# Kernel tuning notes

Measured on AMD Instinct MI355X. Metric: run time of the kernel, lower is better.

The kernel has to match this reference:

```python
import jax, jax.numpy as jnp
import numpy as np

N_HEADS = 16
LN_EPS = 1e-5


def setup_inputs() -> dict:
    key = jax.random.key(0)
    k_z, k_qkv, k_proj = jax.random.split(key, 3)
    b, n, dm = 4, 2048, 1024
    z = jax.random.normal(k_z, (b, n, dm), dtype=jnp.float32)
    gamma = jnp.ones((dm,), dtype=jnp.float32)
    beta = jnp.zeros((dm,), dtype=jnp.float32)
    # parameterize Linear weights as (in, out) so y = x @ w (same math as torch x @ W.T)
    w_qkv = jax.random.normal(k_qkv, (dm, 3 * dm), dtype=jnp.float32) * (1.0 / np.sqrt(dm))
    w_proj = jax.random.normal(k_proj, (dm, dm), dtype=jnp.float32) * (1.0 / np.sqrt(dm))
    b_proj = jnp.zeros((dm,), dtype=jnp.float32)
    return {"z": z, "gamma": gamma, "beta": beta, "w_qkv": w_qkv,
            "w_proj": w_proj, "b_proj": b_proj}


def reference(z, gamma, beta, w_qkv, w_proj, b_proj):
    b, n, dm = z.shape
    h = N_HEADS
    d = dm // h
    scaling = jnp.asarray(np.sqrt(dm / h), dtype=z.dtype)

    # LayerNorm over last dim
    mu = jnp.mean(z, axis=-1, keepdims=True)
    var = jnp.mean(jnp.square(z - mu), axis=-1, keepdims=True)
    zn = (z - mu) * jax.lax.rsqrt(var + LN_EPS) * gamma + beta

    qkv = zn @ w_qkv  # [b, n, 3*dm]
    # einops 'b n (h d qkv_n) -> qkv_n b h n d': qkv index is INNERMOST of packed dim
    qkv = qkv.reshape(b, n, h, d, 3)
    q = qkv[..., 0]  # [b, n, h, d]
    k = qkv[..., 1]
    v = qkv[..., 2]

    scores = jnp.einsum('bqhd,bkhd->bhqk', q, k) / scaling  # [b, h, n, n]
    att = jax.nn.softmax(scores, axis=-1)
    out = jnp.einsum('bhqk,bkhd->bqhd', att, v).reshape(b, n, dm)
    out = out @ w_proj + b_proj  # projection (drop_hidden=False); dropout is identity in eval
    return z + out
```

## Files before the change

### kernel.cpp

```cpp
#include <hip/hip_runtime.h>

typedef unsigned short ushort;
typedef unsigned int uint;

typedef __bf16 bf16x8 __attribute__((ext_vector_type(8)));
typedef float floatx4 __attribute__((ext_vector_type(4)));

constexpr int BATCH = 4;
constexpr int SEQ = 2048;
constexpr int DM = 1024;
constexpr int NH = 16;
constexpr int HD = 64;
constexpr int M = BATCH * SEQ;
constexpr int NQKV = 3 * DM;
constexpr float QSCALE = 0.18033688011112042f;

__device__ __forceinline__ ushort f2b(float f) {
    uint x; __builtin_memcpy(&x, &f, 4);
    x += 0x7fffu + ((x >> 16) & 1u);
    return (ushort)(x >> 16);
}

__device__ __forceinline__ void gload16(const ushort* g, ushort* l) {
    __builtin_amdgcn_global_load_lds(
        (const __attribute__((address_space(1))) void*)g,
        (__attribute__((address_space(3))) void*)l, 16, 0, 0);
}

__global__ __launch_bounds__(256) void prep_kernel(
    const float* __restrict__ w_qkv, ushort* __restrict__ wqT,
    const float* __restrict__ w_proj, ushort* __restrict__ wpT,
    const float* __restrict__ z, const float* __restrict__ gamma,
    const float* __restrict__ beta, ushort* __restrict__ zn) {
    __shared__ ushort tile[64][65];
    int id = blockIdx.x;
    int t = threadIdx.x;
    if (id < 1024) {
        int tx = t & 63, ty = t >> 6;
        if (id < 768) {
            int bx = id % 48, by = id / 48;
            int c0 = bx * 64, r0 = by * 64;
#pragma unroll
            for (int i = 0; i < 64; i += 4)
                tile[i + ty][tx] = f2b(w_qkv[(size_t)(r0 + i + ty) * NQKV + c0 + tx]);
            __syncthreads();
#pragma unroll
            for (int i = 0; i < 64; i += 4) {
                int c = c0 + i + ty;
                int cp = (c % 3) * DM + c / 3;
                wqT[(size_t)cp * DM + r0 + tx] = tile[tx][i + ty];
            }
        } else {
            int q = id - 768;
            int c0 = (q % 16) * 64, r0 = (q / 16) * 64;
#pragma unroll
            for (int i = 0; i < 64; i += 4)
                tile[i + ty][tx] = f2b(w_proj[(size_t)(r0 + i + ty) * DM + c0 + tx]);
            __syncthreads();
#pragma unroll
            for (int i = 0; i < 64; i += 4)
                wpT[(size_t)(c0 + i + ty) * DM + r0 + tx] = tile[tx][i + ty];
        }
        return;
    }
    int row = id - 1024;
    float4 v = reinterpret_cast<const float4*>(z + (size_t)row * DM)[t];
    float s = v.x + v.y + v.z + v.w;
    float sq = v.x * v.x + v.y * v.y + v.z * v.z + v.w * v.w;
#pragma unroll
    for (int off = 32; off >= 1; off >>= 1) {
        s  += __shfl_xor(s, off);
        sq += __shfl_xor(sq, off);
    }
    __shared__ float red[8];
    int wave = t >> 6;
    if ((t & 63) == 0) { red[wave] = s; red[wave + 4] = sq; }
    __syncthreads();
    s  = red[0] + red[1] + red[2] + red[3];
    sq = red[4] + red[5] + red[6] + red[7];
    float mean = s * (1.f / DM);
    float var  = sq * (1.f / DM) - mean * mean;
    float rstd = rsqrtf(var + 1e-5f);
    float4 g = reinterpret_cast<const float4*>(gamma)[t];
    float4 bt = reinterpret_cast<const float4*>(beta)[t];
    ushort4 o;
    o.x = f2b((v.x - mean) * rstd * g.x + bt.x);
    o.y = f2b((v.y - mean) * rstd * g.y + bt.y);
    o.z = f2b((v.z - mean) * rstd * g.z + bt.z);
    o.w = f2b((v.w - mean) * rstd * g.w + bt.w);
    reinterpret_cast<ushort4*>(zn + (size_t)row * DM)[t] = o;
}

__device__ __forceinline__ void gemm128_core(
    const ushort* __restrict__ A, const ushort* __restrict__ BT,
    int m0, int n0, int t, floatx4 (&acc)[4][4],
    ushort (*As)[64], ushort (*Bs)[64]) {
    int lane = t & 63, w = t >> 6;
    int l16 = lane & 15, quad = lane >> 4;
    int wm = (w >> 1) * 64, wn = (w & 1) * 64;
#pragma unroll
    for (int i = 0; i < 4; i++)
#pragma unroll
        for (int j = 0; j < 4; j++) acc[i][j] = (floatx4){0.f, 0.f, 0.f, 0.f};

    int srow8 = lane >> 3;
    int lseg = (lane & 7) ^ srow8;
    const ushort* gA[4]; const ushort* gB[4];
    ushort* lA[4]; ushort* lB[4];
#pragma unroll
    for (int c = 0; c < 4; c++) {
        int r = 32 * c + 8 * w + srow8;
        gA[c] = &A [(size_t)(m0 + r) * DM + lseg * 8];
        gB[c] = &BT[(size_t)(n0 + r) * DM + lseg * 8];
        lA[c] = &As[32 * c + 8 * w][0];
        lB[c] = &Bs[32 * c + 8 * w][0];
    }
    int sw = l16 & 7;

    for (int k0 = 0; k0 < DM; k0 += 64) {
#pragma unroll
        for (int c = 0; c < 4; c++) {
            gload16(gA[c] + k0, lA[c]);
            gload16(gB[c] + k0, lB[c]);
        }
        __syncthreads();
#pragma unroll
        for (int kk = 0; kk < 2; kk++) {
            bf16x8 af[4], bf[4];
#pragma unroll
            for (int i = 0; i < 4; i++)
                af[i] = *reinterpret_cast<const bf16x8*>(
                    &As[wm + i * 16 + l16][((kk * 4 + quad) ^ sw) << 3]);
#pragma unroll
            for (int j = 0; j < 4; j++)
                bf[j] = *reinterpret_cast<const bf16x8*>(
                    &Bs[wn + j * 16 + l16][((kk * 4 + quad) ^ sw) << 3]);
#pragma unroll
            for (int i = 0; i < 4; i++)
#pragma unroll
                for (int j = 0; j < 4; j++)
                    acc[i][j] = __builtin_amdgcn_mfma_f32_16x16x32_bf16(
                        af[i], bf[j], acc[i][j], 0, 0, 0);
        }
        __syncthreads();
    }
}

__global__ __launch_bounds__(256) void gemm_qkv(
    const ushort* __restrict__ A,
    const ushort* __restrict__ BT,
    ushort* __restrict__ Q, ushort* __restrict__ K, ushort* __restrict__ V) {
    __shared__ ushort smem[16384];
    ushort (*As)[64] = (ushort(*)[64])smem;
    ushort (*Bs)[64] = (ushort(*)[64])(smem + 8192);
    ushort* Cs = smem;
    int t = threadIdx.x;
    int id = blockIdx.x;
    int m0 = (id & 63) * 128, n0 = (id >> 6) * 128;
    floatx4 acc[4][4];
    gemm128_core(A, BT, m0, n0, t, acc, As, Bs);
    int lane = t & 63, w = t >> 6;
    int l16 = lane & 15, quad = lane >> 4;
    int wn = (w & 1) * 64;
    int which = n0 >> 10;
    int hd0 = n0 & 1023;
    float scale = (which == 0) ? QSCALE : 1.0f;
    int bb = m0 >> 11;
    int nb = m0 & 2047;
    ushort* dstQK = (which == 0) ? Q : K;

#pragma unroll
    for (int p = 0; p < 2; p++) {
        __syncthreads();
        if ((w >> 1) == p) {
            if (which < 2) {
#pragma unroll
                for (int i = 0; i < 4; i++)
#pragma unroll
                    for (int j = 0; j < 4; j++)
#pragma unroll
                        for (int r = 0; r < 4; r++)
                            Cs[(i * 16 + quad * 4 + r) * 136 + wn + j * 16 + l16] =
                                f2b(acc[i][j][r] * scale);
            } else {
#pragma unroll
                for (int i = 0; i < 4; i++)
#pragma unroll
                    for (int j = 0; j < 4; j++)
#pragma unroll
                        for (int r = 0; r < 4; r++)
                            Cs[(wn + j * 16 + l16) * 72 + i * 16 + quad * 4 + r] =
                                f2b(acc[i][j][r]);
            }
        }
        __syncthreads();
        if (which < 2) {
            int ch = (t & 15) * 8;
#pragma unroll
            for (int u = 0; u < 4; u++) {
                int lr = (t >> 4) + u * 16;
                int n = nb + p * 64 + lr;
                int hh = (hd0 + ch) >> 6, dd = ch & 63;
                *reinterpret_cast<uint4*>(
                    &dstQK[((size_t)((bb * NH + hh) * SEQ) + n) * HD + dd]) =
                    *reinterpret_cast<const uint4*>(&Cs[lr * 136 + ch]);
            }
        } else {
            int nch = (t & 7) * 8;
#pragma unroll
            for (int u = 0; u < 4; u++) {
                int dc = (t >> 3) + u * 32;
                int hh = (hd0 >> 6) + (dc >> 6), dd = dc & 63;
                int n = nb + p * 64 + nch;
                *reinterpret_cast<uint4*>(
                    &V[((size_t)((bb * NH + hh) * HD) + dd) * SEQ + n]) =
                    *reinterpret_cast<const uint4*>(&Cs[dc * 72 + nch]);
            }
        }
    }
}

__global__ __launch_bounds__(256) void gemm_proj(
    const ushort* __restrict__ A,
    const ushort* __restrict__ BT,
    const float* __restrict__ bias, const float* __restrict__ z,
    float* __restrict__ out) {
    __shared__ ushort As[128][64];
    __shared__ ushort Bs[128][64];
    int t = threadIdx.x;
    int id = blockIdx.x;
    int m0 = (id & 63) * 128, n0 = (id >> 6) * 128;
    floatx4 acc[4][4];
    gemm128_core(A, BT, m0, n0, t, acc, As, Bs);
    int lane = t & 63, w = t >> 6;
    int l16 = lane & 15, quad = lane >> 4;
    int wm = (w >> 1) * 64, wn = (w & 1) * 64;
#pragma unroll
    for (int j = 0; j < 4; j++) {
        int col = n0 + wn + j * 16 + l16;
        float bz = bias[col];
#pragma unroll
        for (int i = 0; i < 4; i++) {
#pragma unroll
            for (int r = 0; r < 4; r++) {
                int row = m0 + wm + i * 16 + quad * 4 + r;
                out[(size_t)row * DM + col] =
                    acc[i][j][r] + bz + z[(size_t)row * DM + col];
            }
        }
    }
}

__global__ __launch_bounds__(256) void attn_kernel(
    const ushort* __restrict__ Q, const ushort* __restrict__ K,
    const ushort* __restrict__ Vt, ushort* __restrict__ O) {
    __shared__ ushort QsPs[128 * 64];
    __shared__ ushort Ks[64 * 64];
    __shared__ ushort Vs[64 * 64];
    int t = threadIdx.x;
    int lane = t & 63, w = t >> 6;
    int l16 = lane & 15, quad = lane >> 4;
    int id = blockIdx.x;
    int qt = id >> 6, bh = id & 63;
    int bb = bh >> 4, h = bh & 15;
    int q0 = qt * 128;
    const ushort* Qg = Q  + (size_t)((bb * NH + h) * SEQ + q0) * HD;
    const ushort* Kg = K  + (size_t)((bb * NH + h) * SEQ) * HD;
    const ushort* Vg = Vt + (size_t)((bb * NH + h) * HD) * SEQ;

    int srow = lane >> 3;
    int lseg = (lane & 7) ^ srow;
    int r0 = 8 * w + srow;

    gload16(Qg + (size_t)r0 * HD + lseg * 8,         &QsPs[w * 512]);
    gload16(Qg + (size_t)(32 + r0) * HD + lseg * 8,  &QsPs[2048 + w * 512]);
    gload16(Qg + (size_t)(64 + r0) * HD + lseg * 8,  &QsPs[4096 + w * 512]);
    gload16(Qg + (size_t)(96 + r0) * HD + lseg * 8,  &QsPs[6144 + w * 512]);
    gload16(Kg + (size_t)r0 * HD + lseg * 8,         &Ks[w * 512]);
    gload16(Kg + (size_t)(32 + r0) * HD + lseg * 8,  &Ks[2048 + w * 512]);
    gload16(Vg + (size_t)r0 * SEQ + lseg * 8,        &Vs[w * 512]);
    gload16(Vg + (size_t)(32 + r0) * SEQ + lseg * 8, &Vs[2048 + w * 512]);
    __syncthreads();

    int swl = l16 & 7;
    int hi4 = (l16 >> 3) << 2;
    bf16x8 aq[2][2];
    ushort* PsRow[2];
#pragma unroll
    for (int g = 0; g < 2; g++) {
        int row = 32 * w + 16 * g + l16;
        aq[g][0] = *reinterpret_cast<const bf16x8*>(&QsPs[row * 64 + ((quad ^ swl) << 3)]);
        aq[g][1] = *reinterpret_cast<const bf16x8*>(&QsPs[row * 64 + (((quad + 4) ^ swl) << 3)]);
        PsRow[g] = &QsPs[row * 64];
    }

    size_t koff1 = (size_t)r0 * HD + lseg * 8;
    size_t koff2 = (size_t)(32 + r0) * HD + lseg * 8;
    size_t voff1 = (size_t)r0 * SEQ + lseg * 8;
    size_t voff2 = (size_t)(32 + r0) * SEQ + lseg * 8;
    ushort* kw1 = &Ks[w * 512 + (lane & 63) * 8];
    ushort* kw2 = &Ks[2048 + w * 512 + (lane & 63) * 8];
    ushort* vw1 = &Vs[w * 512 + (lane & 63) * 8];
    ushort* vw2 = &Vs[2048 + w * 512 + (lane & 63) * 8];
    const ushort* Kp = Kg + (size_t)64 * HD;
    const ushort* Vp = Vg + 64;

    bf16x8 bones;
    {
        union { ushort u[8]; bf16x8 v; } cvt;
        ushort one = (l16 == 0) ? (ushort)0x3F80 : (ushort)0;
#pragma unroll
        for (int i = 0; i < 8; i++) cvt.u[i] = one;
        bones = cvt.v;
    }

    floatx4 Oacc[2][4], lacc[2];
#pragma unroll
    for (int g = 0; g < 2; g++) {
        lacc[g] = (floatx4){0.f, 0.f, 0.f, 0.f};
#pragma unroll
        for (int tt = 0; tt < 4; tt++) Oacc[g][tt] = (floatx4){0.f, 0.f, 0.f, 0.f};
    }

    constexpr int NT = SEQ / 64;
    for (int kt = 0; kt < NT; kt++) {
        uint4 kr1 = *reinterpret_cast<const uint4*>(Kp + koff1);
        uint4 kr2 = *reinterpret_cast<const uint4*>(Kp + koff2);
        uint4 vr1 = *reinterpret_cast<const uint4*>(Vp + voff1);
        uint4 vr2 = *reinterpret_cast<const uint4*>(Vp + voff2);
        Kp += (size_t)64 * HD;
        Vp += 64;

        floatx4 sacc[2][4];
#pragma unroll
        for (int nt = 0; nt < 4; nt++) {
            bf16x8 ak0 = *reinterpret_cast<const bf16x8*>(&Ks[(nt * 16 + l16) * 64 + ((quad ^ swl) << 3)]);
            bf16x8 ak1 = *reinterpret_cast<const bf16x8*>(&Ks[(nt * 16 + l16) * 64 + (((quad + 4) ^ swl) << 3)]);
#pragma unroll
            for (int g = 0; g < 2; g++) {
                floatx4 sv = (floatx4){0.f, 0.f, 0.f, 0.f};
                sv = __builtin_amdgcn_mfma_f32_16x16x32_bf16(ak0, aq[g][0], sv, 0, 0, 0);
                sv = __builtin_amdgcn_mfma_f32_16x16x32_bf16(ak1, aq[g][1], sv, 0, 0, 0);
                sacc[g][nt] = sv;
            }
        }
#pragma unroll
        for (int g = 0; g < 2; g++) {
#pragma unroll
            for (int nt = 0; nt < 4; nt++) {
                float p0 = __builtin_amdgcn_exp2f(sacc[g][nt][0]);
                float p1 = __builtin_amdgcn_exp2f(sacc[g][nt][1]);
                float p2 = __builtin_amdgcn_exp2f(sacc[g][nt][2]);
                float p3 = __builtin_amdgcn_exp2f(sacc[g][nt][3]);
                uint b0, b1, b2, b3;
                __builtin_memcpy(&b0, &p0, 4); __builtin_memcpy(&b1, &p1, 4);
                __builtin_memcpy(&b2, &p2, 4); __builtin_memcpy(&b3, &p3, 4);
                uint2 pk;
                pk.x = __builtin_amdgcn_perm(b1, b0, 0x07060302u);
                pk.y = __builtin_amdgcn_perm(b3, b2, 0x07060302u);
                int lseg2 = 2 * nt + (quad >> 1);
                *reinterpret_cast<uint2*>(
                    &PsRow[g][((lseg2 ^ swl ^ hi4) << 3) + (quad & 1) * 4]) = pk;
            }
        }
#pragma unroll
        for (int ks = 0; ks < 2; ks++) {
            bf16x8 ap[2];
#pragma unroll
            for (int g = 0; g < 2; g++) {
                ap[g] = *reinterpret_cast<const bf16x8*>(
                    &PsRow[g][(((4 * ks + quad) ^ swl ^ hi4) << 3)]);
                lacc[g] = __builtin_amdgcn_mfma_f32_16x16x32_bf16(ap[g], bones, lacc[g], 0, 0, 0);
            }
#pragma unroll
            for (int tt = 0; tt < 4; tt++) {
                bf16x8 bv = *reinterpret_cast<const bf16x8*>(
                    &Vs[(tt * 16 + l16) * 64 + ((((ks * 4 + quad)) ^ swl) << 3)]);
#pragma unroll
                for (int g = 0; g < 2; g++)
                    Oacc[g][tt] = __builtin_amdgcn_mfma_f32_16x16x32_bf16(ap[g], bv, Oacc[g][tt], 0, 0, 0);
            }
        }
        __syncthreads();
        *reinterpret_cast<uint4*>(kw1) = kr1;
        *reinterpret_cast<uint4*>(kw2) = kr2;
        *reinterpret_cast<uint4*>(vw1) = vr1;
        *reinterpret_cast<uint4*>(vw2) = vr2;
        __syncthreads();
    }
    float lq[2][4];
#pragma unroll
    for (int g = 0; g < 2; g++)
#pragma unroll
        for (int j = 0; j < 4; j++) lq[g][j] = __shfl(lacc[g][j], quad << 4);

#pragma unroll
    for (int g = 0; g < 2; g++) {
#pragma unroll
        for (int tt = 0; tt < 4; tt++) {
#pragma unroll
            for (int j = 0; j < 4; j++) {
                int n = q0 + 32 * w + 16 * g + quad * 4 + j;
                int dcol = tt * 16 + l16;
                float val = Oacc[g][tt][j] / lq[g][j];
                O[(size_t)(bb * SEQ + n) * DM + h * HD + dcol] = f2b(val);
            }
        }
    }
}

extern "C" void kernel_launch(void* const* d_in, const int* in_sizes, int n_in,
                              void* d_out, int out_size, void* d_ws, size_t ws_size,
                              hipStream_t stream) {
    const float* z      = (const float*)d_in[0];
    const float* gamma  = (const float*)d_in[1];
    const float* beta   = (const float*)d_in[2];
    const float* w_qkv  = (const float*)d_in[3];
    const float* w_proj = (const float*)d_in[4];
    const float* b_proj = (const float*)d_in[5];
    float* out = (float*)d_out;

    char* ws = (char*)d_ws;
    const size_t SZ = (size_t)M * DM * sizeof(ushort);
    ushort* zn   = (ushort*)(ws);
    ushort* Qb   = (ushort*)(ws + SZ);
    ushort* Kb   = (ushort*)(ws + 2 * SZ);
    ushort* Vb   = (ushort*)(ws + 3 * SZ);
    ushort* wqT  = (ushort*)(ws + 4 * SZ);
    ushort* wpT  = (ushort*)(ws + 4 * SZ + (size_t)DM * NQKV * sizeof(ushort));
    ushort* Ob = zn;

    prep_kernel<<<1024 + M, 256, 0, stream>>>(w_qkv, wqT, w_proj, wpT,
                                              z, gamma, beta, zn);
    gemm_qkv<<<(NQKV / 128) * 64, 256, 0, stream>>>(zn, wqT, Qb, Kb, Vb);
    attn_kernel<<<(SEQ / 128) * BATCH * NH, 256, 0, stream>>>(Qb, Kb, Vb, Ob);
    gemm_proj<<<(DM / 128) * 64, 256, 0, stream>>>(Ob, wpT, b_proj, z, out);
}
```

Baseline: 273.0 us.

## Halve attention KV tile to 32 keys and shrink shared memory footprint

The attention kernel now walks keys in 32-row tiles instead of 64, shrinking the K, V and P shared buffers to a total of 16 KB, with the Q staging reusing these buffers once before the loop. New XOR swizzles are introduced for the narrower V and P layouts. The aim is more resident blocks per CU and fewer prefetch registers per thread. In exchange the loop runs twice as many iterations, each with two barriers and less MFMA work to hide global load latency.

```diff
diff --git a/kernel.cpp b/kernel.cpp
--- a/kernel.cpp
+++ b/kernel.cpp
@@ -254,9 +254,9 @@
 __global__ __launch_bounds__(256) void attn_kernel(
     const ushort* __restrict__ Q, const ushort* __restrict__ K,
     const ushort* __restrict__ Vt, ushort* __restrict__ O) {
-    __shared__ ushort QsPs[128 * 64];
-    __shared__ ushort Ks[64 * 64];
-    __shared__ ushort Vs[64 * 64];
+    __shared__ ushort Ps[128 * 32];
+    __shared__ ushort Ks[32 * 64];
+    __shared__ ushort Vs[64 * 32];
     int t = threadIdx.x;
     int lane = t & 63, w = t >> 6;
     int l16 = lane & 15, quad = lane >> 4;
@@ -271,39 +271,41 @@
     int srow = lane >> 3;
     int lseg = (lane & 7) ^ srow;
     int r0 = 8 * w + srow;
-
-    gload16(Qg + (size_t)r0 * HD + lseg * 8,         &QsPs[w * 512]);
-    gload16(Qg + (size_t)(32 + r0) * HD + lseg * 8,  &QsPs[2048 + w * 512]);
-    gload16(Qg + (size_t)(64 + r0) * HD + lseg * 8,  &QsPs[4096 + w * 512]);
-    gload16(Qg + (size_t)(96 + r0) * HD + lseg * 8,  &QsPs[6144 + w * 512]);
-    gload16(Kg + (size_t)r0 * HD + lseg * 8,         &Ks[w * 512]);
-    gload16(Kg + (size_t)(32 + r0) * HD + lseg * 8,  &Ks[2048 + w * 512]);
-    gload16(Vg + (size_t)r0 * SEQ + lseg * 8,        &Vs[w * 512]);
-    gload16(Vg + (size_t)(32 + r0) * SEQ + lseg * 8, &Vs[2048 + w * 512]);
+    int rv = 16 * w + (lane >> 2);
+    int mv = ((lane >> 2) & 3) ^ quad;
+    int sv = (lane & 3) ^ mv;
+
+    gload16(Qg + (size_t)r0 * HD + lseg * 8,         &Ps[w * 512]);
+    gload16(Qg + (size_t)(32 + r0) * HD + lseg * 8,  &Ps[2048 + w * 512]);
+    gload16(Qg + (size_t)(64 + r0) * HD + lseg * 8,  &Ks[w * 512]);
+    gload16(Qg + (size_t)(96 + r0) * HD + lseg * 8,  &Vs[w * 512]);
     __syncthreads();
 
     int swl = l16 & 7;
-    int hi4 = (l16 >> 3) << 2;
+    int swp = l16 & 6;
+    int mvr = (l16 & 3) ^ ((l16 >> 2) & 3);
     bf16x8 aq[2][2];
-    ushort* PsRow[2];
-#pragma unroll
-    for (int g = 0; g < 2; g++) {
-        int row = 32 * w + 16 * g + l16;
-        aq[g][0] = *reinterpret_cast<const bf16x8*>(&QsPs[row * 64 + ((quad ^ swl) << 3)]);
-        aq[g][1] = *reinterpret_cast<const bf16x8*>(&QsPs[row * 64 + (((quad + 4) ^ swl) << 3)]);
-        PsRow[g] = &QsPs[row * 64];
-    }
-
-    size_t koff1 = (size_t)r0 * HD + lseg * 8;
-    size_t koff2 = (size_t)(32 + r0) * HD + lseg * 8;
-    size_t voff1 = (size_t)r0 * SEQ + lseg * 8;
-    size_t voff2 = (size_t)(32 + r0) * SEQ + lseg * 8;
-    ushort* kw1 = &Ks[w * 512 + (lane & 63) * 8];
-    ushort* kw2 = &Ks[2048 + w * 512 + (lane & 63) * 8];
-    ushort* vw1 = &Vs[w * 512 + (lane & 63) * 8];
-    ushort* vw2 = &Vs[2048 + w * 512 + (lane & 63) * 8];
-    const ushort* Kp = Kg + (size_t)64 * HD;
-    const ushort* Vp = Vg + 64;
+    {
+        const ushort* qb = (w == 0) ? Ps : (w == 1) ? (Ps + 2048)
+                          : (w == 2) ? Ks : Vs;
+#pragma unroll
+        for (int g = 0; g < 2; g++) {
+            int rr = 16 * g + l16;
+            aq[g][0] = *reinterpret_cast<const bf16x8*>(&qb[rr * 64 + ((quad ^ swl) << 3)]);
+            aq[g][1] = *reinterpret_cast<const bf16x8*>(&qb[rr * 64 + (((quad + 4) ^ swl) << 3)]);
+        }
+    }
+    __syncthreads();
+    gload16(Kg + (size_t)r0 * HD + lseg * 8, &Ks[w * 512]);
+    gload16(Vg + (size_t)rv * SEQ + sv * 8,  &Vs[w * 512]);
+    __syncthreads();
+
+    size_t koff = (size_t)r0 * HD + lseg * 8;
+    size_t voff = (size_t)rv * SEQ + sv * 8;
+    ushort* kw = &Ks[w * 512 + lane * 8];
+    ushort* vw = &Vs[w * 512 + lane * 8];
+    const ushort* Kp = Kg + (size_t)32 * HD;
+    const ushort* Vp = Vg + 32;
 
     bf16x8 bones;
     {
@@ -314,6 +316,11 @@
         bones = cvt.v;
     }
 
+    ushort* PsRow[2];
+#pragma unroll
+    for (int g = 0; g < 2; g++)
+        PsRow[g] = &Ps[(32 * w + 16 * g + l16) * 32];
+
     floatx4 Oacc[2][4], lacc[2];
 #pragma unroll
     for (int g = 0; g < 2; g++) {
@@ -322,32 +329,30 @@
         for (int tt = 0; tt < 4; tt++) Oacc[g][tt] = (floatx4){0.f, 0.f, 0.f, 0.f};
     }
 
-    constexpr int NT = SEQ / 64;
+    constexpr int NT = SEQ / 32;
     for (int kt = 0; kt < NT; kt++) {
-        uint4 kr1 = *reinterpret_cast<const uint4*>(Kp + koff1);
-        uint4 kr2 = *reinterpret_cast<const uint4*>(Kp + koff2);
-        uint4 vr1 = *reinterpret_cast<const uint4*>(Vp + voff1);
-        uint4 vr2 = *reinterpret_cast<const uint4*>(Vp + voff2);
-        Kp += (size_t)64 * HD;
-        Vp += 64;
-
-        floatx4 sacc[2][4];
-#pragma unroll
-        for (int nt = 0; nt < 4; nt++) {
+        uint4 kr = *reinterpret_cast<const uint4*>(Kp + koff);
+        uint4 vr = *reinterpret_cast<const uint4*>(Vp + voff);
+        Kp += (size_t)32 * HD;
+        Vp += 32;
+
+        floatx4 sacc[2][2];
+#pragma unroll
+        for (int nt = 0; nt < 2; nt++) {
             bf16x8 ak0 = *reinterpret_cast<const bf16x8*>(&Ks[(nt * 16 + l16) * 64 + ((quad ^ swl) << 3)]);
             bf16x8 ak1 = *reinterpret_cast<const bf16x8*>(&Ks[(nt * 16 + l16) * 64 + (((quad + 4) ^ swl) << 3)]);
 #pragma unroll
             for (int g = 0; g < 2; g++) {
-                floatx4 sv = (floatx4){0.f, 0.f, 0.f, 0.f};
-                sv = __builtin_amdgcn_mfma_f32_16x16x32_bf16(ak0, aq[g][0], sv, 0, 0, 0);
-                sv = __builtin_amdgcn_mfma_f32_16x16x32_bf16(ak1, aq[g][1], sv, 0, 0, 0);
-                sacc[g][nt] = sv;
+                floatx4 sv2 = (floatx4){0.f, 0.f, 0.f, 0.f};
+                sv2 = __builtin_amdgcn_mfma_f32_16x16x32_bf16(ak0, aq[g][0], sv2, 0, 0, 0);
+                sv2 = __builtin_amdgcn_mfma_f32_16x16x32_bf16(ak1, aq[g][1], sv2, 0, 0, 0);
+                sacc[g][nt] = sv2;
             }
         }
 #pragma unroll
         for (int g = 0; g < 2; g++) {
 #pragma unroll
-            for (int nt = 0; nt < 4; nt++) {
+            for (int nt = 0; nt < 2; nt++) {
                 float p0 = __builtin_amdgcn_exp2f(sacc[g][nt][0]);
                 float p1 = __builtin_amdgcn_exp2f(sacc[g][nt][1]);
                 float p2 = __builtin_amdgcn_exp2f(sacc[g][nt][2]);
@@ -358,34 +363,28 @@
                 uint2 pk;
                 pk.x = __builtin_amdgcn_perm(b1, b0, 0x07060302u);
                 pk.y = __builtin_amdgcn_perm(b3, b2, 0x07060302u);
-                int lseg2 = 2 * nt + (quad >> 1);
                 *reinterpret_cast<uint2*>(
-                    &PsRow[g][((lseg2 ^ swl ^ hi4) << 3) + (quad & 1) * 4]) = pk;
-            }
-        }
-#pragma unroll
-        for (int ks = 0; ks < 2; ks++) {
-            bf16x8 ap[2];
-#pragma unroll
-            for (int g = 0; g < 2; g++) {
-                ap[g] = *reinterpret_cast<const bf16x8*>(
-                    &PsRow[g][(((4 * ks + quad) ^ swl ^ hi4) << 3)]);
-                lacc[g] = __builtin_amdgcn_mfma_f32_16x16x32_bf16(ap[g], bones, lacc[g], 0, 0, 0);
-            }
-#pragma unroll
-            for (int tt = 0; tt < 4; tt++) {
-                bf16x8 bv = *reinterpret_cast<const bf16x8*>(
-                    &Vs[(tt * 16 + l16) * 64 + ((((ks * 4 + quad)) ^ swl) << 3)]);
-#pragma unroll
-                for (int g = 0; g < 2; g++)
-                    Oacc[g][tt] = __builtin_amdgcn_mfma_f32_16x16x32_bf16(ap[g], bv, Oacc[g][tt], 0, 0, 0);
-            }
-        }
-        __syncthreads();
-        *reinterpret_cast<uint4*>(kw1) = kr1;
-        *reinterpret_cast<uint4*>(kw2) = kr2;
-        *reinterpret_cast<uint4*>(vw1) = vr1;
-        *reinterpret_cast<uint4*>(vw2) = vr2;
+                    &PsRow[g][((nt * 4 + quad) ^ swp) * 4]) = pk;
+            }
+        }
+        bf16x8 ap[2];
+#pragma unroll
+        for (int g = 0; g < 2; g++) {
+            ap[g] = *reinterpret_cast<const bf16x8*>(
+                &PsRow[g][((2 * quad) ^ swp) * 4]);
+            lacc[g] = __builtin_amdgcn_mfma_f32_16x16x32_bf16(ap[g], bones, lacc[g], 0, 0, 0);
+        }
+#pragma unroll
+        for (int tt = 0; tt < 4; tt++) {
+            bf16x8 bv = *reinterpret_cast<const bf16x8*>(
+                &Vs[(tt * 16 + l16) * 32 + ((quad ^ mvr) << 3)]);
+#pragma unroll
+            for (int g = 0; g < 2; g++)
+                Oacc[g][tt] = __builtin_amdgcn_mfma_f32_16x16x32_bf16(ap[g], bv, Oacc[g][tt], 0, 0, 0);
+        }
+        __syncthreads();
+        *reinterpret_cast<uint4*>(kw) = kr;
+        *reinterpret_cast<uint4*>(vw) = vr;
         __syncthreads();
     }
     float lq[2][4];
```

Result: slower. 281.4 us (+3.0%).
